# Kernel optimization log

Hardware: AMD Instinct MI355X
Metric: run time of the kernel (lower is better)

The kernel has to match this reference:

```python
import jax, jax.numpy as jnp
import numpy as np

B, S, H = 2, 2048, 2048
NH = 16
HD = H // NH          # 128
ROT = HD // 4         # rotary_dim = head_dim * 0.25 = 32
VP = 320              # v_proj_dim
BASE = 10000.0


def setup_inputs() -> dict:
    key = jax.random.key(0)
    ks = jax.random.split(key, 10)
    sc = lambda fan_in: 1.0 / np.sqrt(fan_in)
    return {
        "hidden_states": jax.random.normal(ks[0], (B, S, H), jnp.float32),
        "Wqkv": jax.random.normal(ks[1], (3 * H, H), jnp.float32) * sc(H),
        "bqkv": jnp.zeros((3 * H,), jnp.float32),
        "Wc": jax.random.normal(ks[2], (VP, H), jnp.float32) * sc(H),
        "bc": jnp.zeros((VP,), jnp.float32),
        "Wr": jax.random.normal(ks[3], (H, VP), jnp.float32) * sc(VP),
        "br": jnp.zeros((H,), jnp.float32),
        "Wd": jax.random.normal(ks[4], (H, H), jnp.float32) * sc(H),
        "bd": jnp.zeros((H,), jnp.float32),
    }


def _rope_tables(seq_len, rot_dim, dtype):
    inv_freq = 1.0 / (BASE ** (jnp.arange(0, rot_dim, 2, dtype=jnp.float32) / rot_dim))
    t = jnp.arange(seq_len, dtype=jnp.float32)
    freqs = jnp.outer(t, inv_freq)                      # [S, rot/2]
    emb = jnp.concatenate([freqs, freqs], axis=-1)      # [S, rot]
    return jnp.cos(emb).astype(dtype), jnp.sin(emb).astype(dtype)


def _rotate_half(x):
    x1, x2 = jnp.split(x, 2, axis=-1)
    return jnp.concatenate([-x2, x1], axis=-1)


def reference(hidden_states, Wqkv, bqkv, Wc, bc, Wr, br, Wd, bd):
    b, s, h = hidden_states.shape
    qkv = hidden_states @ Wqkv.T + bqkv                 # [B,S,3H]
    qkv = qkv.reshape(b, s, 3, NH, HD)
    qkv = jnp.transpose(qkv, (2, 0, 3, 1, 4))           # [3,B,NH,S,HD]
    q, k, v = qkv[0], qkv[1], qkv[2]

    cos, sin = _rope_tables(s, ROT, hidden_states.dtype)  # [S,ROT]
    cos = cos[None, None, :, :]
    sin = sin[None, None, :, :]
    q_rot, q_pass = q[..., :ROT], q[..., ROT:]
    k_rot, k_pass = k[..., :ROT], k[..., ROT:]
    q_rot = q_rot * cos + _rotate_half(q_rot) * sin
    k_rot = k_rot * cos + _rotate_half(k_rot) * sin
    q = jnp.concatenate([q_rot, q_pass], axis=-1)
    k = jnp.concatenate([k_rot, k_pass], axis=-1)

    # V low-rank compress / restore
    v_hidden = jnp.transpose(v, (0, 2, 1, 3)).reshape(b, s, h)  # [B,S,H]
    v_restored = (v_hidden @ Wc.T + bc) @ Wr.T + br             # [B,S,H]
    v_heads = jnp.transpose(v_restored.reshape(b, s, NH, HD), (0, 2, 1, 3))  # [B,NH,S,HD]

    scale = HD ** -0.5
    scores = jnp.einsum('bhqd,bhkd->bhqk', q, k) * scale
    causal = jnp.triu(jnp.full((s, s), -jnp.inf, scores.dtype), k=1)
    scores = scores + causal
    attn = jax.nn.softmax(scores, axis=-1)
    out = jnp.einsum('bhqk,bhkd->bhqd', attn, v_heads)
    out = jnp.transpose(out, (0, 2, 1, 3)).reshape(b, s, h)
    return out @ Wd.T + bd
```

## Files before the change

### kernel.cpp

```cpp
#include <hip/hip_runtime.h>

typedef unsigned short u16;
typedef unsigned int u32;
typedef __bf16 bf16x8 __attribute__((ext_vector_type(8)));
typedef float f32x4 __attribute__((ext_vector_type(4)));

#define BB 2
#define SS 2048
#define HH 2048
#define NHH 16
#define HDD 128

__device__ __forceinline__ float b2f(u16 u) {
  union { u32 i; float f; } v; v.i = ((u32)u) << 16; return v.f;
}
__device__ __forceinline__ u16 f2b(float f) {
  union { float f; u32 i; } v; v.f = f;
  u32 x = v.i;
  u32 r = (x + 0x7fffu + ((x >> 16) & 1u)) >> 16;
  return (u16)r;
}

__device__ __forceinline__ void gload_lds16(const u16* g, u16* l) {
  __builtin_amdgcn_global_load_lds(
      (const __attribute__((address_space(1))) u32*)g,
      (__attribute__((address_space(3))) u32*)l, 16, 0, 0);
}

__global__ __launch_bounds__(256) void cvt_kernel(
    const float* __restrict__ s0, u16* __restrict__ d0, int n0,
    const float* __restrict__ s1, u16* __restrict__ d1, int n1,
    const float* __restrict__ s2, u16* __restrict__ d2, int n2,
    const float* __restrict__ s3, u16* __restrict__ d3, int n3,
    const float* __restrict__ s4, u16* __restrict__ d4, int n4)
{
  const float* s; u16* d; int n;
  switch (blockIdx.y) {
    case 0: s = s0; d = d0; n = n0; break;
    case 1: s = s1; d = d1; n = n1; break;
    case 2: s = s2; d = d2; n = n2; break;
    case 3: s = s3; d = d3; n = n3; break;
    default: s = s4; d = d4; n = n4; break;
  }
  int nq = n >> 2;
  for (int q = blockIdx.x * 256 + threadIdx.x; q < nq; q += gridDim.x * 256) {
    float4 v = *(const float4*)(s + (size_t)q * 4);
    ushort4 o;
    o.x = f2b(v.x); o.y = f2b(v.y); o.z = f2b(v.z); o.w = f2b(v.w);
    *(ushort4*)(d + (size_t)q * 4) = o;
  }
}

template<int OUT_F32>
__global__ __launch_bounds__(256) void gemm_bias_kernel(
    const u16* __restrict__ A, const u16* __restrict__ Bw,
    const float* __restrict__ bias, void* __restrict__ Cv,
    int M, int N, int K, int lda, int ldb, int ldc)
{
  __shared__ u16 Asf[128 * 4 * 8];
  __shared__ u16 Bsf[128 * 4 * 8];
  const int t = threadIdx.x;
  const int m0 = blockIdx.y * 128;
  const int n0 = blockIdx.x * 128;
  const int lane = t & 63, wid = t >> 6;
  const int wm = (wid >> 1) * 64, wn = (wid & 1) * 64;
  const int quad = lane >> 4, lm = lane & 15;

  const int r16 = lane >> 2;
  const int swz = ((lane >> 2) & 3) ^ ((lane >> 4) & 3);
  const int kc = ((lane & 3) ^ swz) * 8;
  const int fswz = (lm & 3) ^ ((lm >> 2) & 3);

  f32x4 acc[4][4] = {};

  for (int k0 = 0; k0 < K; k0 += 32) {
    __syncthreads();
#pragma unroll
    for (int it = 0; it < 2; ++it) {
      int g = wid * 2 + it;
      int r = g * 16 + r16;
      gload_lds16(A + (size_t)(m0 + r) * lda + k0 + kc, &Asf[(size_t)g * 512]);
      gload_lds16(Bw + (size_t)(n0 + r) * ldb + k0 + kc, &Bsf[(size_t)g * 512]);
    }
    __syncthreads();
    bf16x8 af[4], bf[4];
#pragma unroll
    for (int i = 0; i < 4; ++i) {
      int row = wm + i * 16 + lm;
      af[i] = *(const bf16x8*)&Asf[(size_t)(row * 4 + (quad ^ fswz)) * 8];
    }
#pragma unroll
    for (int j = 0; j < 4; ++j) {
      int row = wn + j * 16 + lm;
      bf[j] = *(const bf16x8*)&Bsf[(size_t)(row * 4 + (quad ^ fswz)) * 8];
    }
#pragma unroll
    for (int i = 0; i < 4; ++i)
#pragma unroll
      for (int j = 0; j < 4; ++j)
        acc[i][j] = __builtin_amdgcn_mfma_f32_16x16x32_bf16(af[i], bf[j], acc[i][j], 0, 0, 0);
  }

#pragma unroll
  for (int i = 0; i < 4; ++i) {
    int gm = m0 + wm + i * 16 + quad * 4;
#pragma unroll
    for (int j = 0; j < 4; ++j) {
      int gn = n0 + wn + j * 16 + lm;
      if (gn < N) {
        float bsv = bias[gn];
        f32x4 a = acc[i][j];
        if (OUT_F32) {
          float* C = (float*)Cv;
#pragma unroll
          for (int rg = 0; rg < 4; ++rg)
            C[(size_t)(gm + rg) * ldc + gn] = a[rg] + bsv;
        } else {
          u16* C = (u16*)Cv;
#pragma unroll
          for (int rg = 0; rg < 4; ++rg)
            C[(size_t)(gm + rg) * ldc + gn] = f2b(a[rg] + bsv);
        }
      }
    }
  }
}

__global__ __launch_bounds__(256) void rope_kernel(u16* __restrict__ qkv)
{
  int idx = blockIdx.x * 256 + threadIdx.x;
  int i = idx & 15;
  int h = (idx >> 4) & 15;
  int rs = idx >> 8;
  int s = rs & (SS - 1);
  float inv_freq = exp2f(-(float)i * 0.8304820237218406f);
  float ang = (float)s * inv_freq;
  float sn, c;
  sincosf(ang, &sn, &c);
  size_t base = (size_t)rs * 6144 + (size_t)h * 128;
  {
    float x0 = b2f(qkv[base + i]), x1 = b2f(qkv[base + i + 16]);
    qkv[base + i]      = f2b(x0 * c - x1 * sn);
    qkv[base + i + 16] = f2b(x1 * c + x0 * sn);
  }
  {
    size_t kb = base + 2048;
    float x0 = b2f(qkv[kb + i]), x1 = b2f(qkv[kb + i + 16]);
    qkv[kb + i]      = f2b(x0 * c - x1 * sn);
    qkv[kb + i + 16] = f2b(x1 * c + x0 * sn);
  }
}

__global__ __launch_bounds__(256) void transpose_v_kernel(const u16* __restrict__ vr,
                                                          u16* __restrict__ vrt)
{
  __shared__ u16 L[64][72];
  const int t = threadIdx.x;
  const int s0 = blockIdx.x * 64;
  const int d0 = blockIdx.y * 64;
  const int bh = blockIdx.z; const int b = bh >> 4, h = bh & 15;
#pragma unroll
  for (int it = 0; it < 2; ++it) {
    int c = t + it * 256;
    int sl = c >> 3, d8 = c & 7;
    *(uint4*)&L[sl][d8 * 8] =
      *(const uint4*)(vr + (size_t)(b * 2048 + s0 + sl) * 2048 + h * 128 + d0 + d8 * 8);
  }
  __syncthreads();
#pragma unroll
  for (int it = 0; it < 2; ++it) {
    int c = t + it * 256;
    int d = c >> 3, s8 = c & 7;
    u16 tmp[8];
#pragma unroll
    for (int r = 0; r < 8; ++r) tmp[r] = L[s8 * 8 + r][d];
    uint4 o;
    o.x = (u32)tmp[0] | ((u32)tmp[1] << 16);
    o.y = (u32)tmp[2] | ((u32)tmp[3] << 16);
    o.z = (u32)tmp[4] | ((u32)tmp[5] << 16);
    o.w = (u32)tmp[6] | ((u32)tmp[7] << 16);
    *(uint4*)(vrt + ((size_t)bh * 128 + d0 + d) * 2048 + s0 + s8 * 8) = o;
  }
}

__global__ __launch_bounds__(256) void attn_mfma_kernel(
    const u16* __restrict__ qkv, const u16* __restrict__ vrt, u16* __restrict__ out)
{
  __shared__ u16 Kt[64 * 16 * 8];
  __shared__ u16 Vt[8][128][8];
  __shared__ u16 Pa[4][8][16][8];

  const int t = threadIdx.x;
  const int lane = t & 63, w = t >> 6;
  const int quad = lane >> 4, lm = lane & 15;
  const int bx = blockIdx.x;
  const int bh = bx & 31;
  const int qt = 31 - (bx >> 5);
  const int b = bh >> 4, h = bh & 15;
  const int q0 = qt * 64;
  const int qw = q0 + w * 16;

  bf16x8 qf[4];
  {
    const u16* qsrc = qkv + (size_t)(b * SS + qw + lm) * 6144 + h * 128 + quad * 8;
#pragma unroll
    for (int dc = 0; dc < 4; ++dc) qf[dc] = *(const bf16x8*)(qsrc + dc * 32);
  }

  f32x4 Oa[8] = {};
  float mrow[4], lrow[4];
#pragma unroll
  for (int r = 0; r < 4; ++r) { mrow[r] = -1e30f; lrow[r] = 0.f; }

  const float scale = 0.08838834764831845f;
  const int nkt = qt + 1;
  const u16* kbase = qkv + (size_t)b * SS * 6144 + 2048 + h * 128;
  const u16* vbase = vrt + (size_t)bh * 128 * 2048;

  for (int kt = 0; kt < nkt; ++kt) {
    const int kb = kt * 64;
    __syncthreads();
#pragma unroll
    for (int it = 0; it < 4; ++it) {
      int c = t + it * 256;
      int kp = c >> 4, dq = c & 15;
      *(uint4*)&Kt[(size_t)(kp * 16 + (dq ^ (kp & 15))) * 8] =
          *(const uint4*)(kbase + (size_t)(kb + kp) * 6144 + dq * 8);
      int d = c >> 3, kq = c & 7;
      *(uint4*)&Vt[kq][d][0] =
          *(const uint4*)(vbase + (size_t)d * 2048 + kb + kq * 8);
    }
    __syncthreads();

    f32x4 sa[4] = {};
#pragma unroll
    for (int ct = 0; ct < 4; ++ct) {
#pragma unroll
      for (int dc = 0; dc < 4; ++dc) {
        bf16x8 kf = *(const bf16x8*)&Kt[(size_t)((ct * 16 + lm) * 16 +
                                                 ((dc * 4 + quad) ^ lm)) * 8];
        sa[ct] = __builtin_amdgcn_mfma_f32_16x16x32_bf16(qf[dc], kf, sa[ct], 0, 0, 0);
      }
    }
#pragma unroll
    for (int ct = 0; ct < 4; ++ct)
#pragma unroll
      for (int r = 0; r < 4; ++r) sa[ct][r] *= scale;

    if (kt == nkt - 1) {
#pragma unroll
      for (int ct = 0; ct < 4; ++ct) {
        int kpos = kb + ct * 16 + lm;
#pragma unroll
        for (int r = 0; r < 4; ++r)
          if (kpos > qw + quad * 4 + r) sa[ct][r] = -1e30f;
      }
    }

    float alpha[4];
#pragma unroll
    for (int r = 0; r < 4; ++r) {
      float mx = fmaxf(fmaxf(sa[0][r], sa[1][r]), fmaxf(sa[2][r], sa[3][r]));
#pragma unroll
      for (int off = 1; off < 16; off <<= 1)
        mx = fmaxf(mx, __shfl_xor(mx, off, 64));
      float mnew = fmaxf(mrow[r], mx);
      alpha[r] = __expf(mrow[r] - mnew);
      float s = 0.f;
#pragma unroll
      for (int ct = 0; ct < 4; ++ct) {
        float p = __expf(sa[ct][r] - mnew);
        sa[ct][r] = p;
        s += p;
      }
#pragma unroll
      for (int off = 1; off < 16; off <<= 1)
        s += __shfl_xor(s, off, 64);
      lrow[r] = lrow[r] * alpha[r] + s;
      mrow[r] = mnew;
    }

#pragma unroll
    for (int dt = 0; dt < 8; ++dt)
#pragma unroll
      for (int r = 0; r < 4; ++r) Oa[dt][r] *= alpha[r];

#pragma unroll
    for (int ct = 0; ct < 4; ++ct) {
      int kq = ct * 2 + (lm >> 3), j = lm & 7;
#pragma unroll
      for (int r = 0; r < 4; ++r)
        Pa[w][kq][quad * 4 + r][j] = f2b(sa[ct][r]);
    }
    bf16x8 pf0 = *(const bf16x8*)&Pa[w][quad][lm][0];
    bf16x8 pf1 = *(const bf16x8*)&Pa[w][4 + quad][lm][0];

#pragma unroll
    for (int dt = 0; dt < 8; ++dt) {
      bf16x8 vf0 = *(const bf16x8*)&Vt[quad][dt * 16 + lm][0];
      bf16x8 vf1 = *(const bf16x8*)&Vt[4 + quad][dt * 16 + lm][0];
      Oa[dt] = __builtin_amdgcn_mfma_f32_16x16x32_bf16(pf0, vf0, Oa[dt], 0, 0, 0);
      Oa[dt] = __builtin_amdgcn_mfma_f32_16x16x32_bf16(pf1, vf1, Oa[dt], 0, 0, 0);
    }
  }

  float inv[4];
#pragma unroll
  for (int r = 0; r < 4; ++r) inv[r] = 1.0f / lrow[r];
  u16* dst = out + (size_t)(b * SS + qw + quad * 4) * 2048 + h * 128 + lm;
#pragma unroll
  for (int r = 0; r < 4; ++r)
#pragma unroll
    for (int dt = 0; dt < 8; ++dt)
      dst[(size_t)r * 2048 + dt * 16] = f2b(Oa[dt][r] * inv[r]);
}

extern "C" void kernel_launch(void* const* d_in, const int* in_sizes, int n_in,
                              void* d_out, int out_size, void* d_ws, size_t ws_size,
                              hipStream_t stream)
{
  (void)in_sizes; (void)n_in; (void)out_size; (void)ws_size;
  const float* X    = (const float*)d_in[0];
  const float* Wqkv = (const float*)d_in[1];
  const float* bqkv = (const float*)d_in[2];
  const float* Wc   = (const float*)d_in[3];
  const float* bc   = (const float*)d_in[4];
  const float* Wr   = (const float*)d_in[5];
  const float* br   = (const float*)d_in[6];
  const float* Wd   = (const float*)d_in[7];
  const float* bd   = (const float*)d_in[8];
  float* out = (float*)d_out;

  char* ws = (char*)d_ws;
  u16* QKV   = (u16*)(ws);
  u16* Xb    = (u16*)(ws + 50331648);
  u16* Vr    = (u16*)(ws + 50331648);
  u16* AO    = (u16*)(ws + 50331648);
  u16* Wqkvb = (u16*)(ws + 67108864);
  u16* VrT   = (u16*)(ws + 67108864);
  u16* Wcb   = (u16*)(ws + 92274688);
  u16* Wrb   = (u16*)(ws + 93585408);
  u16* Cb    = (u16*)(ws + 94896128);
  u16* Wdb   = (u16*)(ws + 97517568);

  dim3 blk(256);

  cvt_kernel<<<dim3(512, 5), blk, 0, stream>>>(
      X, Xb, 4096 * 2048,
      Wqkv, Wqkvb, 6144 * 2048,
      Wc, Wcb, 320 * 2048,
      Wr, Wrb, 2048 * 320,
      Wd, Wdb, 2048 * 2048);

  gemm_bias_kernel<0><<<dim3(48, 32), blk, 0, stream>>>(Xb, Wqkvb, bqkv, QKV,
                                                        4096, 6144, 2048, 2048, 2048, 6144);
  rope_kernel<<<dim3(4096), blk, 0, stream>>>(QKV);
  gemm_bias_kernel<0><<<dim3(3, 32), blk, 0, stream>>>(QKV + 4096, Wcb, bc, Cb,
                                                       4096, 320, 2048, 6144, 2048, 320);
  gemm_bias_kernel<0><<<dim3(16, 32), blk, 0, stream>>>(Cb, Wrb, br, Vr,
                                                        4096, 2048, 320, 320, 320, 2048);
  transpose_v_kernel<<<dim3(32, 2, 32), blk, 0, stream>>>(Vr, VrT);
  attn_mfma_kernel<<<dim3(1024), blk, 0, stream>>>(QKV, VrT, AO);
  gemm_bias_kernel<1><<<dim3(16, 32), blk, 0, stream>>>(AO, Wdb, bd, out,
                                                        4096, 2048, 2048, 2048, 2048, 2048);
}
```

Measured before the change: 539.4 us.

## Fuse RoPE into QKV GEMM epilogue, emit transposed V directly, transpose score MFMA

Applies rotary embedding in the QKV GEMM epilogue, which removes the separate rope kernel. The V-restore GEMM now computes Wr·Cᵀ per batch through a new z-stride, so it writes V already transposed and the transpose kernel goes away. The attention kernel swaps the MFMA operands so each lane owns one query row, which cuts the softmax row reductions to two shuffles, and it packs P stores with a swizzle. The costs are extra sincos work in the GEMM epilogue, and in the restore GEMM, row-bias loads and bf16 stores that are strided across rows rather than contiguous.

Measured after the change: 506.9 us. 6.0% less time.

```diff
diff --git a/kernel.cpp b/kernel.cpp
--- a/kernel.cpp
+++ b/kernel.cpp
@@ -51,11 +51,12 @@
   }
 }
 
-template<int OUT_F32>
+template<int OUT_F32, int ROPE, int BIAS_ROW>
 __global__ __launch_bounds__(256) void gemm_bias_kernel(
     const u16* __restrict__ A, const u16* __restrict__ Bw,
     const float* __restrict__ bias, void* __restrict__ Cv,
-    int M, int N, int K, int lda, int ldb, int ldc)
+    int M, int N, int K, int lda, int ldb, int ldc,
+    size_t strideB, size_t strideC)
 {
   __shared__ u16 Asf[128 * 4 * 8];
   __shared__ u16 Bsf[128 * 4 * 8];
@@ -66,6 +67,8 @@
   const int wm = (wid >> 1) * 64, wn = (wid & 1) * 64;
   const int quad = lane >> 4, lm = lane & 15;
 
+  const u16* Bz = Bw + (size_t)blockIdx.z * strideB;
+
   const int r16 = lane >> 2;
   const int swz = ((lane >> 2) & 3) ^ ((lane >> 4) & 3);
   const int kc = ((lane & 3) ^ swz) * 8;
@@ -80,7 +83,7 @@
       int g = wid * 2 + it;
       int r = g * 16 + r16;
       gload_lds16(A + (size_t)(m0 + r) * lda + k0 + kc, &Asf[(size_t)g * 512]);
-      gload_lds16(Bw + (size_t)(n0 + r) * ldb + k0 + kc, &Bsf[(size_t)g * 512]);
+      gload_lds16(Bz + (size_t)(n0 + r) * ldb + k0 + kc, &Bsf[(size_t)g * 512]);
     }
     __syncthreads();
     bf16x8 af[4], bf[4];
@@ -101,85 +104,43 @@
         acc[i][j] = __builtin_amdgcn_mfma_f32_16x16x32_bf16(af[i], bf[j], acc[i][j], 0, 0, 0);
   }
 
+  float* Cf = (float*)Cv + (OUT_F32 ? (size_t)blockIdx.z * strideC : 0);
+  u16* Cu = (u16*)Cv + (OUT_F32 ? 0 : (size_t)blockIdx.z * strideC);
+  const float ropefreq = ROPE ? exp2f(-(float)lm * 0.8304820237218406f) : 0.f;
+  const bool do_rope = ROPE && (wn == 0) && (n0 < 4096);
+
 #pragma unroll
   for (int i = 0; i < 4; ++i) {
     int gm = m0 + wm + i * 16 + quad * 4;
+    int jstart = 0;
+    if (do_rope) {
+      jstart = 2;
+      int gn0 = n0 + lm, gn1 = gn0 + 16;
+      float b0 = bias[gn0], b1 = bias[gn1];
+#pragma unroll
+      for (int rg = 0; rg < 4; ++rg) {
+        int rs = gm + rg;
+        float sn, cs;
+        sincosf((float)(rs & (SS - 1)) * ropefreq, &sn, &cs);
+        float x0 = acc[i][0][rg] + b0, x1 = acc[i][1][rg] + b1;
+        Cu[(size_t)rs * ldc + gn0] = f2b(x0 * cs - x1 * sn);
+        Cu[(size_t)rs * ldc + gn1] = f2b(x1 * cs + x0 * sn);
+      }
+    }
 #pragma unroll
     for (int j = 0; j < 4; ++j) {
+      if (j < jstart) continue;
       int gn = n0 + wn + j * 16 + lm;
       if (gn < N) {
-        float bsv = bias[gn];
         f32x4 a = acc[i][j];
-        if (OUT_F32) {
-          float* C = (float*)Cv;
-#pragma unroll
-          for (int rg = 0; rg < 4; ++rg)
-            C[(size_t)(gm + rg) * ldc + gn] = a[rg] + bsv;
-        } else {
-          u16* C = (u16*)Cv;
-#pragma unroll
-          for (int rg = 0; rg < 4; ++rg)
-            C[(size_t)(gm + rg) * ldc + gn] = f2b(a[rg] + bsv);
+#pragma unroll
+        for (int rg = 0; rg < 4; ++rg) {
+          float bsv = BIAS_ROW ? bias[gm + rg] : bias[gn];
+          if (OUT_F32) Cf[(size_t)(gm + rg) * ldc + gn] = a[rg] + bsv;
+          else         Cu[(size_t)(gm + rg) * ldc + gn] = f2b(a[rg] + bsv);
         }
       }
     }
-  }
-}
-
-__global__ __launch_bounds__(256) void rope_kernel(u16* __restrict__ qkv)
-{
-  int idx = blockIdx.x * 256 + threadIdx.x;
-  int i = idx & 15;
-  int h = (idx >> 4) & 15;
-  int rs = idx >> 8;
-  int s = rs & (SS - 1);
-  float inv_freq = exp2f(-(float)i * 0.8304820237218406f);
-  float ang = (float)s * inv_freq;
-  float sn, c;
-  sincosf(ang, &sn, &c);
-  size_t base = (size_t)rs * 6144 + (size_t)h * 128;
-  {
-    float x0 = b2f(qkv[base + i]), x1 = b2f(qkv[base + i + 16]);
-    qkv[base + i]      = f2b(x0 * c - x1 * sn);
-    qkv[base + i + 16] = f2b(x1 * c + x0 * sn);
-  }
-  {
-    size_t kb = base + 2048;
-    float x0 = b2f(qkv[kb + i]), x1 = b2f(qkv[kb + i + 16]);
-    qkv[kb + i]      = f2b(x0 * c - x1 * sn);
-    qkv[kb + i + 16] = f2b(x1 * c + x0 * sn);
-  }
-}
-
-__global__ __launch_bounds__(256) void transpose_v_kernel(const u16* __restrict__ vr,
-                                                          u16* __restrict__ vrt)
-{
-  __shared__ u16 L[64][72];
-  const int t = threadIdx.x;
-  const int s0 = blockIdx.x * 64;
-  const int d0 = blockIdx.y * 64;
-  const int bh = blockIdx.z; const int b = bh >> 4, h = bh & 15;
-#pragma unroll
-  for (int it = 0; it < 2; ++it) {
-    int c = t + it * 256;
-    int sl = c >> 3, d8 = c & 7;
-    *(uint4*)&L[sl][d8 * 8] =
-      *(const uint4*)(vr + (size_t)(b * 2048 + s0 + sl) * 2048 + h * 128 + d0 + d8 * 8);
-  }
-  __syncthreads();
-#pragma unroll
-  for (int it = 0; it < 2; ++it) {
-    int c = t + it * 256;
-    int d = c >> 3, s8 = c & 7;
-    u16 tmp[8];
-#pragma unroll
-    for (int r = 0; r < 8; ++r) tmp[r] = L[s8 * 8 + r][d];
-    uint4 o;
-    o.x = (u32)tmp[0] | ((u32)tmp[1] << 16);
-    o.y = (u32)tmp[2] | ((u32)tmp[3] << 16);
-    o.z = (u32)tmp[4] | ((u32)tmp[5] << 16);
-    o.w = (u32)tmp[6] | ((u32)tmp[7] << 16);
-    *(uint4*)(vrt + ((size_t)bh * 128 + d0 + d) * 2048 + s0 + s8 * 8) = o;
   }
 }
 
@@ -188,7 +149,7 @@
 {
   __shared__ u16 Kt[64 * 16 * 8];
   __shared__ u16 Vt[8][128][8];
-  __shared__ u16 Pa[4][8][16][8];
+  __shared__ u16 Pa[4][16 * 64];
 
   const int t = threadIdx.x;
   const int lane = t & 63, w = t >> 6;
@@ -208,14 +169,13 @@
   }
 
   f32x4 Oa[8] = {};
-  float mrow[4], lrow[4];
-#pragma unroll
-  for (int r = 0; r < 4; ++r) { mrow[r] = -1e30f; lrow[r] = 0.f; }
+  float m_i = -1e30f, l_i = 0.f;
 
   const float scale = 0.08838834764831845f;
   const int nkt = qt + 1;
   const u16* kbase = qkv + (size_t)b * SS * 6144 + 2048 + h * 128;
   const u16* vbase = vrt + (size_t)bh * 128 * 2048;
+  u16* pw = &Pa[w][0];
 
   for (int kt = 0; kt < nkt; ++kt) {
     const int kb = kt * 64;
@@ -239,7 +199,7 @@
       for (int dc = 0; dc < 4; ++dc) {
         bf16x8 kf = *(const bf16x8*)&Kt[(size_t)((ct * 16 + lm) * 16 +
                                                  ((dc * 4 + quad) ^ lm)) * 8];
-        sa[ct] = __builtin_amdgcn_mfma_f32_16x16x32_bf16(qf[dc], kf, sa[ct], 0, 0, 0);
+        sa[ct] = __builtin_amdgcn_mfma_f32_16x16x32_bf16(kf, qf[dc], sa[ct], 0, 0, 0);
       }
     }
 #pragma unroll
@@ -248,52 +208,56 @@
       for (int r = 0; r < 4; ++r) sa[ct][r] *= scale;
 
     if (kt == nkt - 1) {
+      int qpos = qw + lm;
 #pragma unroll
       for (int ct = 0; ct < 4; ++ct) {
-        int kpos = kb + ct * 16 + lm;
 #pragma unroll
         for (int r = 0; r < 4; ++r)
-          if (kpos > qw + quad * 4 + r) sa[ct][r] = -1e30f;
-      }
-    }
-
-    float alpha[4];
-#pragma unroll
-    for (int r = 0; r < 4; ++r) {
-      float mx = fmaxf(fmaxf(sa[0][r], sa[1][r]), fmaxf(sa[2][r], sa[3][r]));
-#pragma unroll
-      for (int off = 1; off < 16; off <<= 1)
-        mx = fmaxf(mx, __shfl_xor(mx, off, 64));
-      float mnew = fmaxf(mrow[r], mx);
-      alpha[r] = __expf(mrow[r] - mnew);
-      float s = 0.f;
-#pragma unroll
-      for (int ct = 0; ct < 4; ++ct) {
+          if (kb + ct * 16 + quad * 4 + r > qpos) sa[ct][r] = -1e30f;
+      }
+    }
+
+    float mx = sa[0][0];
+#pragma unroll
+    for (int ct = 0; ct < 4; ++ct)
+#pragma unroll
+      for (int r = 0; r < 4; ++r) mx = fmaxf(mx, sa[ct][r]);
+    mx = fmaxf(mx, __shfl_xor(mx, 16, 64));
+    mx = fmaxf(mx, __shfl_xor(mx, 32, 64));
+    float mnew = fmaxf(m_i, mx);
+    float alpha = __expf(m_i - mnew);
+    float ssum = 0.f;
+#pragma unroll
+    for (int ct = 0; ct < 4; ++ct)
+#pragma unroll
+      for (int r = 0; r < 4; ++r) {
         float p = __expf(sa[ct][r] - mnew);
         sa[ct][r] = p;
-        s += p;
-      }
-#pragma unroll
-      for (int off = 1; off < 16; off <<= 1)
-        s += __shfl_xor(s, off, 64);
-      lrow[r] = lrow[r] * alpha[r] + s;
-      mrow[r] = mnew;
-    }
-
+        ssum += p;
+      }
+    ssum += __shfl_xor(ssum, 16, 64);
+    ssum += __shfl_xor(ssum, 32, 64);
+    l_i = l_i * alpha + ssum;
+    m_i = mnew;
+
+    float ar[4];
+#pragma unroll
+    for (int r = 0; r < 4; ++r) ar[r] = __shfl(alpha, quad * 4 + r, 64);
 #pragma unroll
     for (int dt = 0; dt < 8; ++dt)
 #pragma unroll
-      for (int r = 0; r < 4; ++r) Oa[dt][r] *= alpha[r];
+      for (int r = 0; r < 4; ++r) Oa[dt][r] *= ar[r];
 
 #pragma unroll
     for (int ct = 0; ct < 4; ++ct) {
-      int kq = ct * 2 + (lm >> 3), j = lm & 7;
-#pragma unroll
-      for (int r = 0; r < 4; ++r)
-        Pa[w][kq][quad * 4 + r][j] = f2b(sa[ct][r]);
-    }
-    bf16x8 pf0 = *(const bf16x8*)&Pa[w][quad][lm][0];
-    bf16x8 pf1 = *(const bf16x8*)&Pa[w][4 + quad][lm][0];
+      uint2 pk;
+      pk.x = (u32)f2b(sa[ct][0]) | ((u32)f2b(sa[ct][1]) << 16);
+      pk.y = (u32)f2b(sa[ct][2]) | ((u32)f2b(sa[ct][3]) << 16);
+      int u = ct * 2 + (quad >> 1);
+      *(uint2*)(pw + lm * 64 + ((u ^ (lm & 7)) * 8) + (quad & 1) * 4) = pk;
+    }
+    bf16x8 pf0 = *(const bf16x8*)(pw + lm * 64 + ((quad ^ (lm & 7)) * 8));
+    bf16x8 pf1 = *(const bf16x8*)(pw + lm * 64 + (((4 + quad) ^ (lm & 7)) * 8));
 
 #pragma unroll
     for (int dt = 0; dt < 8; ++dt) {
@@ -304,15 +268,16 @@
     }
   }
 
-  float inv[4];
-#pragma unroll
-  for (int r = 0; r < 4; ++r) inv[r] = 1.0f / lrow[r];
+  float inv = 1.0f / l_i;
+  float ir[4];
+#pragma unroll
+  for (int r = 0; r < 4; ++r) ir[r] = __shfl(inv, quad * 4 + r, 64);
   u16* dst = out + (size_t)(b * SS + qw + quad * 4) * 2048 + h * 128 + lm;
 #pragma unroll
   for (int r = 0; r < 4; ++r)
 #pragma unroll
     for (int dt = 0; dt < 8; ++dt)
-      dst[(size_t)r * 2048 + dt * 16] = f2b(Oa[dt][r] * inv[r]);
+      dst[(size_t)r * 2048 + dt * 16] = f2b(Oa[dt][r] * ir[r]);
 }
 
 extern "C" void kernel_launch(void* const* d_in, const int* in_sizes, int n_in,
@@ -334,7 +299,6 @@
   char* ws = (char*)d_ws;
   u16* QKV   = (u16*)(ws);
   u16* Xb    = (u16*)(ws + 50331648);
-  u16* Vr    = (u16*)(ws + 50331648);
   u16* AO    = (u16*)(ws + 50331648);
   u16* Wqkvb = (u16*)(ws + 67108864);
   u16* VrT   = (u16*)(ws + 67108864);
@@ -352,15 +316,14 @@
       Wr, Wrb, 2048 * 320,
       Wd, Wdb, 2048 * 2048);
 
-  gemm_bias_kernel<0><<<dim3(48, 32), blk, 0, stream>>>(Xb, Wqkvb, bqkv, QKV,
-                                                        4096, 6144, 2048, 2048, 2048, 6144);
-  rope_kernel<<<dim3(4096), blk, 0, stream>>>(QKV);
-  gemm_bias_kernel<0><<<dim3(3, 32), blk, 0, stream>>>(QKV + 4096, Wcb, bc, Cb,
-                                                       4096, 320, 2048, 6144, 2048, 320);
-  gemm_bias_kernel<0><<<dim3(16, 32), blk, 0, stream>>>(Cb, Wrb, br, Vr,
-                                                        4096, 2048, 320, 320, 320, 2048);
-  transpose_v_kernel<<<dim3(32, 2, 32), blk, 0, stream>>>(Vr, VrT);
+  gemm_bias_kernel<0, 1, 0><<<dim3(48, 32), blk, 0, stream>>>(
+      Xb, Wqkvb, bqkv, QKV, 4096, 6144, 2048, 2048, 2048, 6144, 0, 0);
+  gemm_bias_kernel<0, 0, 0><<<dim3(3, 32), blk, 0, stream>>>(
+      QKV + 4096, Wcb, bc, Cb, 4096, 320, 2048, 6144, 2048, 320, 0, 0);
+  gemm_bias_kernel<0, 0, 1><<<dim3(16, 16, 2), blk, 0, stream>>>(
+      Wrb, Cb, br, VrT, 2048, 2048, 320, 320, 320, 2048,
+      (size_t)2048 * 320, (size_t)4194304);
   attn_mfma_kernel<<<dim3(1024), blk, 0, stream>>>(QKV, VrT, AO);
-  gemm_bias_kernel<1><<<dim3(16, 32), blk, 0, stream>>>(AO, Wdb, bd, out,
-                                                        4096, 2048, 2048, 2048, 2048, 2048);
-}
+  gemm_bias_kernel<1, 0, 0><<<dim3(16, 32), blk, 0, stream>>>(
+      AO, Wdb, bd, out, 4096, 2048, 2048, 2048, 2048, 2048, 0, 0);
+}
```
